# Optimization experiments

Measured on AMD Instinct MI355X. Metric: run time of the kernel, lower is better.

The kernel has to match this reference:

```python
import jax, jax.numpy as jnp
import numpy as np

B, C, IN, H = 64, 128, 1024, 512  # batch, channels, input features (=='seq_length' arg), hidden


def setup_inputs() -> dict:
    key = jax.random.key(0)
    ks = jax.random.split(key, 9)
    s = 1.0 / np.sqrt(H)  # PyTorch LSTM init: U(-1/sqrt(H), 1/sqrt(H))
    u = lambda k, shape: jax.random.uniform(k, shape, jnp.float32, -s, s)
    return {
        "x": jax.random.normal(ks[0], (B, C, IN), jnp.float32),
        # layer 0: one weight set per direction (fwd, bwd)
        "W_ih0": u(ks[1], (2, 4 * H, IN)),
        "W_hh0": u(ks[2], (2, 4 * H, H)),
        "b_ih0": u(ks[3], (2, 4 * H)),
        "b_hh0": u(ks[4], (2, 4 * H)),
        # layers 1..2: input is concat of both directions (2H)
        "W_ih12": u(ks[5], (2, 2, 4 * H, 2 * H)),
        "W_hh12": u(ks[6], (2, 2, 4 * H, H)),
        "b_ih12": u(ks[7], (2, 2, 4 * H)),
        "b_hh12": u(ks[8], (2, 2, 4 * H)),
    }


def _cell(inp, W_ih, b_ih, b_hh):
    # One LSTM step from zero state (h0 = c0 = 0): W_hh @ h0 == 0, f*c0 == 0.
    gates = inp @ W_ih.T + b_ih + b_hh  # [N, 4H]
    i, f, g, o = jnp.split(gates, 4, axis=-1)  # PyTorch gate order: i, f, g, o
    c = jax.nn.sigmoid(i) * jnp.tanh(g)
    return jax.nn.sigmoid(o) * jnp.tanh(c)  # h, shape [N, H]


def reference(x, W_ih0, W_hh0, b_ih0, b_hh0, W_ih12, W_hh12, b_ih12, b_hh12):
    b, c, n = x.shape
    # Each channel is an independent seq-len-1 LSTM call with zero init state,
    # so fold channels into the batch dimension. W_hh* contribute nothing (h0=0).
    xb = x.reshape(b * c, n)
    h = jnp.concatenate(
        [_cell(xb, W_ih0[d], b_ih0[d], b_hh0[d]) for d in range(2)], axis=-1
    )  # [b*c, 2H]
    for l in range(2):  # layers 1 and 2
        h = jnp.concatenate(
            [_cell(h, W_ih12[l, d], b_ih12[l, d], b_hh12[l, d]) for d in range(2)],
            axis=-1,
        )
    return h.reshape(b, c, 2 * H)  # [batch, channels, 2*hidden]
```

## Files before the change

### kernel.cpp

```cpp
#include <hip/hip_runtime.h>


typedef float f32x4 __attribute__((ext_vector_type(4)));
typedef short short8 __attribute__((ext_vector_type(8)));
typedef unsigned short u16;

#define NP 3072
#define MROWS 8192
#define KDIM 1024
#define BM 256
#define BN 192
#define BK 64
#define LDS_A_SZ (BM * BK * 2)
#define LDS_B_SZ (BN * BK * 2)
#define LDS_B_OFF (2 * LDS_A_SZ)

__device__ __forceinline__ u16 f2bf(float f) {
  unsigned u = __float_as_uint(f);
  u += 0x7fffu + ((u >> 16) & 1u);
  return (u16)(u >> 16);
}
__device__ __forceinline__ float sigmoid_f(float x) {
  return 1.0f / (1.0f + __expf(-x));
}
__device__ __forceinline__ float tanh_f(float x) {
  float xc = fminf(fmaxf(x, -15.0f), 15.0f);
  float e = __expf(2.0f * xc);
  return (e - 1.0f) / (e + 1.0f);
}
__device__ __forceinline__ void gload_lds16(const void* g, void* l) {
  __builtin_amdgcn_global_load_lds((const __attribute__((address_space(1))) void*)g,
                                   (__attribute__((address_space(3))) void*)l,
                                   16, 0, 0);
}


__global__ __launch_bounds__(256) void k_convert_x(const float* __restrict__ x,
                                                   u16* __restrict__ out) {
  int tid = blockIdx.x * 256 + threadIdx.x;
  const float4* src = (const float4*)x + (size_t)tid * 2;
  float4 v0 = src[0], v1 = src[1];
  union { u16 u[8]; uint4 v; } r;
  r.u[0] = f2bf(v0.x); r.u[1] = f2bf(v0.y); r.u[2] = f2bf(v0.z); r.u[3] = f2bf(v0.w);
  r.u[4] = f2bf(v1.x); r.u[5] = f2bf(v1.y); r.u[6] = f2bf(v1.z); r.u[7] = f2bf(v1.w);
  ((uint4*)out)[tid] = r.v;
}

__global__ __launch_bounds__(256) void k_pack_w(const float* __restrict__ Wih0,
                                                const float* __restrict__ Wih12,
                                                u16* __restrict__ P) {
  int tid = blockIdx.x * 256 + threadIdx.x;
  int s   = tid / (NP * 128);
  int rem = tid - s * (NP * 128);
  int p   = rem >> 7;
  int k8  = rem & 127;
  int hb = p / 48;
  int pr = p - hb * 48;
  int gs = pr >> 4;
  int hl = pr & 15;
  int hcol = hb * 16 + hl;
  int dir = hcol >> 9;
  int h   = hcol & 511;
  int og  = (gs == 0) ? 0 : (gs + 1);
  const float* src;
  if (s == 0)
    src = Wih0 + ((size_t)(dir * 2048 + og * 512 + h)) * 1024 + k8 * 8;
  else
    src = Wih12 + ((size_t)(((s - 1) * 2 + dir) * 2048 + og * 512 + h)) * 1024 + k8 * 8;
  float4 v0 = ((const float4*)src)[0];
  float4 v1 = ((const float4*)src)[1];
  union { u16 u[8]; uint4 v; } r;
  r.u[0] = f2bf(v0.x); r.u[1] = f2bf(v0.y); r.u[2] = f2bf(v0.z); r.u[3] = f2bf(v0.w);
  r.u[4] = f2bf(v1.x); r.u[5] = f2bf(v1.y); r.u[6] = f2bf(v1.z); r.u[7] = f2bf(v1.w);
  ((uint4*)P)[tid] = r.v;
}

__global__ __launch_bounds__(256) void k_pack_bias(const float* __restrict__ bih0,
                                                   const float* __restrict__ bhh0,
                                                   const float* __restrict__ bih12,
                                                   const float* __restrict__ bhh12,
                                                   float* __restrict__ pb) {
  int tid = blockIdx.x * 256 + threadIdx.x;
  if (tid >= 3 * NP) return;
  int s = tid / NP;
  int p = tid - s * NP;
  int hb = p / 48;
  int pr = p - hb * 48;
  int gs = pr >> 4;
  int hl = pr & 15;
  int hcol = hb * 16 + hl;
  int dir = hcol >> 9;
  int h   = hcol & 511;
  int og  = (gs == 0) ? 0 : (gs + 1);
  int j   = og * 512 + h;
  float v;
  if (s == 0) {
    int i = dir * 2048 + j;
    v = bih0[i] + bhh0[i];
  } else {
    int i = ((s - 1) * 2 + dir) * 2048 + j;
    v = bih12[i] + bhh12[i];
  }
  pb[tid] = v;
}


#define BAR()    __builtin_amdgcn_s_barrier()
#define SCHEDB() __builtin_amdgcn_sched_barrier(0)
#define WAITV(N) asm volatile("s_waitcnt vmcnt(" #N ")" ::: "memory")
#define MM(Macc, Aop, Bop) Macc = __builtin_amdgcn_mfma_f32_16x16x32_bf16(Aop, Bop, Macc, 0, 0, 0)

#define LDA(MQ, K32, M4, BUF) \
  (*(const short8*)(lds + ((K32) ? aK1 : aK0) + ((BUF) * LDS_A_SZ + (MQ) * 8192 + (M4) * 2048)))
#define LDB(N3, K32, BUF) \
  (*(const short8*)(lds + ((K32) ? bK1 : bK0) + ((BUF) * LDS_B_SZ + (N3) * 2048)))

#define STAGE_B(RB, BUF, KT) \
  gload_lds16(srcB + (size_t)(RB) * 64 * KDIM + (size_t)(KT) * BK, \
              lds + LDS_B_OFF + (BUF) * LDS_B_SZ + (RB) * 8192 + t * 16)
#define STAGE_A(ROWB, BUF, KT) \
  gload_lds16(srcA + (size_t)(ROWB) * KDIM + (size_t)(KT) * BK, \
              lds + (BUF) * LDS_A_SZ + (ROWB) * 128 + t * 16)

#define MM12(MQ, AA0, AA1, AA2, AA3, BB0, BB1, BB2) \
  MM(acc[(MQ)*4+0][0], AA0, BB0); MM(acc[(MQ)*4+1][0], AA1, BB0); \
  MM(acc[(MQ)*4+2][0], AA2, BB0); MM(acc[(MQ)*4+3][0], AA3, BB0); \
  MM(acc[(MQ)*4+0][1], AA0, BB1); MM(acc[(MQ)*4+1][1], AA1, BB1); \
  MM(acc[(MQ)*4+2][1], AA2, BB1); MM(acc[(MQ)*4+3][1], AA3, BB1); \
  MM(acc[(MQ)*4+0][2], AA0, BB2); MM(acc[(MQ)*4+1][2], AA1, BB2); \
  MM(acc[(MQ)*4+2][2], AA2, BB2); MM(acc[(MQ)*4+3][2], AA3, BB2);

#define TILE1(BUF, KT, DO_STAGE) \
  { \
    if (DO_STAGE) { STAGE_B(0, (BUF)^1, (KT)+1); STAGE_B(1, (BUF)^1, (KT)+1); STAGE_B(2, (BUF)^1, (KT)+1); \
                    STAGE_A(0, (BUF)^1, (KT)+1); STAGE_A(128, (BUF)^1, (KT)+1); \
                    STAGE_A(64, (BUF)^1, (KT)+1); STAGE_A(192, (BUF)^1, (KT)+1); } \
    SCHEDB(); \
    a0 = LDA(0, 0, 0, BUF); a1 = LDA(0, 0, 1, BUF); a2 = LDA(0, 0, 2, BUF); a3 = LDA(0, 0, 3, BUF); \
    b00 = LDB(0, 0, BUF); b01 = LDB(1, 0, BUF); b02 = LDB(2, 0, BUF); \
    a8 = LDA(1, 0, 0, BUF); a9 = LDA(1, 0, 1, BUF); aA = LDA(1, 0, 2, BUF); aB = LDA(1, 0, 3, BUF); \
    a4 = LDA(0, 1, 0, BUF); a5 = LDA(0, 1, 1, BUF); a6 = LDA(0, 1, 2, BUF); a7 = LDA(0, 1, 3, BUF); \
    b10 = LDB(0, 1, BUF); b11 = LDB(1, 1, BUF); b12 = LDB(2, 1, BUF); \
    aC = LDA(1, 1, 0, BUF); aD = LDA(1, 1, 1, BUF); aE = LDA(1, 1, 2, BUF); aF = LDA(1, 1, 3, BUF); \
    __builtin_amdgcn_s_setprio(1); \
    MM12(0, a0, a1, a2, a3, b00, b01, b02); \
    MM12(1, a8, a9, aA, aB, b00, b01, b02); \
    MM12(0, a4, a5, a6, a7, b10, b11, b12); \
    MM12(1, aC, aD, aE, aF, b10, b11, b12); \
    __builtin_amdgcn_s_setprio(0); \
    WAITV(0); \
    BAR(); SCHEDB(); \
  }

template <bool F32OUT>
__global__ __launch_bounds__(512, 2) void k_lstm_gemm8(const u16* __restrict__ A,
                                                       const u16* __restrict__ Bp,
                                                       const float* __restrict__ bias,
                                                       void* __restrict__ outp) {
  __shared__ __align__(16) char lds[114688];
  const int t    = threadIdx.x;
  const int lane = t & 63;
  const int w    = t >> 6;
  const int wr   = w >> 2;
  const int wc   = w & 3;
  const int r16  = lane & 15, kg = lane >> 4;

  const int n_hw = blockIdx.y * gridDim.x + blockIdx.x;
  const int c    = n_hw & 7;
  const int wlc  = n_hw >> 3;
  const int bx   = (c & 1) * 8 + (wlc & 7);
  const int by   = (c >> 1) * 8 + (wlc >> 3);
  const int brow = by * BM;
  const int bn0  = bx * BN;

  const int sw    = r16 & 7;
  const int slot0 = kg ^ sw;
  const int aK0 = wr * 16384 + r16 * 128 + slot0 * 16;
  const int aK1 = wr * 16384 + r16 * 128 + (slot0 ^ 4) * 16;
  const int bK0 = LDS_B_OFF + (wc * 48 + r16) * 128 + slot0 * 16;
  const int bK1 = LDS_B_OFF + (wc * 48 + r16) * 128 + (slot0 ^ 4) * 16;

  const int rr   = t >> 3;
  const int koct = ((t & 7) ^ (rr & 7)) << 3;
  const u16* srcA = A  + (size_t)(brow + rr) * KDIM + koct;
  const u16* srcB = Bp + (size_t)(bn0  + rr) * KDIM + koct;

  f32x4 acc[8][3];
#pragma unroll
  for (int m = 0; m < 8; ++m)
#pragma unroll
    for (int n = 0; n < 3; ++n) acc[m][n] = (f32x4){0.f, 0.f, 0.f, 0.f};

  short8 a0, a1, a2, a3, a4, a5, a6, a7, a8, a9, aA, aB, aC, aD, aE, aF;
  short8 b00, b01, b02, b10, b11, b12;

  STAGE_B(0, 0, 0); STAGE_B(1, 0, 0); STAGE_B(2, 0, 0);
  STAGE_A(0, 0, 0); STAGE_A(128, 0, 0);
  STAGE_A(64, 0, 0); STAGE_A(192, 0, 0);
  WAITV(0);
  BAR(); SCHEDB();

  for (int k2 = 0; k2 < 7; ++k2) {
    int kt = k2 * 2;
    TILE1(0, kt, 1);
    TILE1(1, kt + 1, 1);
  }
  TILE1(0, 14, 1);
  TILE1(1, 15, 0);

  {
    int pb = bn0 + wc * 48;
    float biV = bias[pb + r16];
    float bgV = bias[pb + 16 + r16];
    float boV = bias[pb + 32 + r16];
    int hcol = (bx * 4 + wc) * 16 + r16;
#pragma unroll
    for (int m8 = 0; m8 < 8; ++m8) {
      int rowb = brow + wr * 128 + (m8 >> 2) * 64 + (m8 & 3) * 16 + kg * 4;
#pragma unroll
      for (int r = 0; r < 4; ++r) {
        float vi = acc[m8][0][r] + biV;
        float vg = acc[m8][1][r] + bgV;
        float vo = acc[m8][2][r] + boV;
        float c2 = sigmoid_f(vi) * tanh_f(vg);
        float hv = sigmoid_f(vo) * tanh_f(c2);
        size_t oidx = (size_t)(rowb + r) * 1024 + hcol;
        if (F32OUT) ((float*)outp)[oidx] = hv;
        else        ((u16*)outp)[oidx]   = f2bf(hv);
      }
    }
  }
}

extern "C" void kernel_launch(void* const* d_in, const int* in_sizes, int n_in,
                              void* d_out, int out_size, void* d_ws, size_t ws_size,
                              hipStream_t stream) {
  const float* x     = (const float*)d_in[0];
  const float* Wih0  = (const float*)d_in[1];
  const float* bih0  = (const float*)d_in[3];
  const float* bhh0  = (const float*)d_in[4];
  const float* Wih12 = (const float*)d_in[5];
  const float* bih12 = (const float*)d_in[7];
  const float* bhh12 = (const float*)d_in[8];

  char* ws = (char*)d_ws;
  u16*   xbf = (u16*)ws;
  u16*   h1  = (u16*)(ws + 16777216);
  u16*   h2  = (u16*)(ws + 33554432);
  u16*   P3  = (u16*)(ws + 50331648);
  float* pb3 = (float*)(ws + 69206016);

  k_convert_x<<<4096, 256, 0, stream>>>(x, xbf);
  k_pack_w<<<4608, 256, 0, stream>>>(Wih0, Wih12, P3);
  k_pack_bias<<<36, 256, 0, stream>>>(bih0, bhh0, bih12, bhh12, pb3);

  dim3 grid(NP / BN, MROWS / BM);
  k_lstm_gemm8<false><<<grid, 512, 0, stream>>>(xbf, P3, pb3, h1);
  k_lstm_gemm8<false><<<grid, 512, 0, stream>>>(h1, P3 + (size_t)NP * KDIM, pb3 + NP, h2);
  k_lstm_gemm8<true ><<<grid, 512, 0, stream>>>(h2, P3 + (size_t)2 * NP * KDIM, pb3 + 2 * NP, d_out);
}
```

Before: 197.3 us.

## Load B operands directly from global into registers, stage only A in LDS

B-matrix fragments are now read straight from global memory into registers, double-buffered across the two K halves, instead of going through LDS. LDS holds only the A tile. Warps are remapped from a 2x4 to a 4x2 grid, so each warp computes 64 rows by 96 columns. This cuts LDS footprint and LDS read traffic, but adds global loads with latency the schedule must hide, raises register pressure, and can lower reuse of B across warps.

```diff
diff --git a/kernel.cpp b/kernel.cpp
--- a/kernel.cpp
+++ b/kernel.cpp
@@ -12,8 +12,6 @@
 #define BN 192
 #define BK 64
 #define LDS_A_SZ (BM * BK * 2)
-#define LDS_B_SZ (BN * BK * 2)
-#define LDS_B_OFF (2 * LDS_A_SZ)
 
 __device__ __forceinline__ u16 f2bf(float f) {
   unsigned u = __float_as_uint(f);
@@ -110,46 +108,54 @@
 #define WAITV(N) asm volatile("s_waitcnt vmcnt(" #N ")" ::: "memory")
 #define MM(Macc, Aop, Bop) Macc = __builtin_amdgcn_mfma_f32_16x16x32_bf16(Aop, Bop, Macc, 0, 0, 0)
 
-#define LDA(MQ, K32, M4, BUF) \
-  (*(const short8*)(lds + ((K32) ? aK1 : aK0) + ((BUF) * LDS_A_SZ + (MQ) * 8192 + (M4) * 2048)))
-#define LDB(N3, K32, BUF) \
-  (*(const short8*)(lds + ((K32) ? bK1 : bK0) + ((BUF) * LDS_B_SZ + (N3) * 2048)))
-
-#define STAGE_B(RB, BUF, KT) \
-  gload_lds16(srcB + (size_t)(RB) * 64 * KDIM + (size_t)(KT) * BK, \
-              lds + LDS_B_OFF + (BUF) * LDS_B_SZ + (RB) * 8192 + t * 16)
+#define LDA0(M4) (*(const short8*)(lds + aK0 + ((M4) * 2048)))
+#define LDA1(M4) (*(const short8*)(lds + aK1 + ((M4) * 2048)))
+#define LDA0B(M4) (*(const short8*)(lds + LDS_A_SZ + aK0 + ((M4) * 2048)))
+#define LDA1B(M4) (*(const short8*)(lds + LDS_A_SZ + aK1 + ((M4) * 2048)))
+
 #define STAGE_A(ROWB, BUF, KT) \
   gload_lds16(srcA + (size_t)(ROWB) * KDIM + (size_t)(KT) * BK, \
               lds + (BUF) * LDS_A_SZ + (ROWB) * 128 + t * 16)
-
-#define MM12(MQ, AA0, AA1, AA2, AA3, BB0, BB1, BB2) \
-  MM(acc[(MQ)*4+0][0], AA0, BB0); MM(acc[(MQ)*4+1][0], AA1, BB0); \
-  MM(acc[(MQ)*4+2][0], AA2, BB0); MM(acc[(MQ)*4+3][0], AA3, BB0); \
-  MM(acc[(MQ)*4+0][1], AA0, BB1); MM(acc[(MQ)*4+1][1], AA1, BB1); \
-  MM(acc[(MQ)*4+2][1], AA2, BB1); MM(acc[(MQ)*4+3][1], AA3, BB1); \
-  MM(acc[(MQ)*4+0][2], AA0, BB2); MM(acc[(MQ)*4+1][2], AA1, BB2); \
-  MM(acc[(MQ)*4+2][2], AA2, BB2); MM(acc[(MQ)*4+3][2], AA3, BB2);
-
-#define TILE1(BUF, KT, DO_STAGE) \
+#define STAGE_A4(BUF, KT) \
+  STAGE_A(0, BUF, KT); STAGE_A(64, BUF, KT); STAGE_A(128, BUF, KT); STAGE_A(192, BUF, KT)
+
+#define BLOAD6(DST, KT, K32) \
+  DST##0 = *(const short8*)(bB + 0 * 16 * KDIM + (KT) * 64 + (K32) * 32); \
+  DST##1 = *(const short8*)(bB + 1 * 16 * KDIM + (KT) * 64 + (K32) * 32); \
+  DST##2 = *(const short8*)(bB + 2 * 16 * KDIM + (KT) * 64 + (K32) * 32); \
+  DST##3 = *(const short8*)(bB + 3 * 16 * KDIM + (KT) * 64 + (K32) * 32); \
+  DST##4 = *(const short8*)(bB + 4 * 16 * KDIM + (KT) * 64 + (K32) * 32); \
+  DST##5 = *(const short8*)(bB + 5 * 16 * KDIM + (KT) * 64 + (K32) * 32)
+
+#define MM24(A0_, A1_, A2_, A3_, BB) \
+  MM(acc[0][0], A0_, BB##0); MM(acc[1][0], A1_, BB##0); MM(acc[2][0], A2_, BB##0); MM(acc[3][0], A3_, BB##0); \
+  MM(acc[0][1], A0_, BB##1); MM(acc[1][1], A1_, BB##1); MM(acc[2][1], A2_, BB##1); MM(acc[3][1], A3_, BB##1); \
+  MM(acc[0][2], A0_, BB##2); MM(acc[1][2], A1_, BB##2); MM(acc[2][2], A2_, BB##2); MM(acc[3][2], A3_, BB##2); \
+  MM(acc[0][3], A0_, BB##3); MM(acc[1][3], A1_, BB##3); MM(acc[2][3], A2_, BB##3); MM(acc[3][3], A3_, BB##3); \
+  MM(acc[0][4], A0_, BB##4); MM(acc[1][4], A1_, BB##4); MM(acc[2][4], A2_, BB##4); MM(acc[3][4], A3_, BB##4); \
+  MM(acc[0][5], A0_, BB##5); MM(acc[1][5], A1_, BB##5); MM(acc[2][5], A2_, BB##5); MM(acc[3][5], A3_, BB##5)
+
+#define TILE(BUF, KT, DO_STAGE) \
   { \
-    if (DO_STAGE) { STAGE_B(0, (BUF)^1, (KT)+1); STAGE_B(1, (BUF)^1, (KT)+1); STAGE_B(2, (BUF)^1, (KT)+1); \
-                    STAGE_A(0, (BUF)^1, (KT)+1); STAGE_A(128, (BUF)^1, (KT)+1); \
-                    STAGE_A(64, (BUF)^1, (KT)+1); STAGE_A(192, (BUF)^1, (KT)+1); } \
-    SCHEDB(); \
-    a0 = LDA(0, 0, 0, BUF); a1 = LDA(0, 0, 1, BUF); a2 = LDA(0, 0, 2, BUF); a3 = LDA(0, 0, 3, BUF); \
-    b00 = LDB(0, 0, BUF); b01 = LDB(1, 0, BUF); b02 = LDB(2, 0, BUF); \
-    a8 = LDA(1, 0, 0, BUF); a9 = LDA(1, 0, 1, BUF); aA = LDA(1, 0, 2, BUF); aB = LDA(1, 0, 3, BUF); \
-    a4 = LDA(0, 1, 0, BUF); a5 = LDA(0, 1, 1, BUF); a6 = LDA(0, 1, 2, BUF); a7 = LDA(0, 1, 3, BUF); \
-    b10 = LDB(0, 1, BUF); b11 = LDB(1, 1, BUF); b12 = LDB(2, 1, BUF); \
-    aC = LDA(1, 1, 0, BUF); aD = LDA(1, 1, 1, BUF); aE = LDA(1, 1, 2, BUF); aF = LDA(1, 1, 3, BUF); \
+    if (DO_STAGE) { STAGE_A4((BUF)^1, (KT)+1); } \
+    SCHEDB(); \
+    BLOAD6(bqA, KT, 1); \
+    SCHEDB(); \
+    if (BUF) { aA0 = LDA0B(0); aA1 = LDA0B(1); aA2 = LDA0B(2); aA3 = LDA0B(3); } \
+    else     { aA0 = LDA0(0);  aA1 = LDA0(1);  aA2 = LDA0(2);  aA3 = LDA0(3);  } \
     __builtin_amdgcn_s_setprio(1); \
-    MM12(0, a0, a1, a2, a3, b00, b01, b02); \
-    MM12(1, a8, a9, aA, aB, b00, b01, b02); \
-    MM12(0, a4, a5, a6, a7, b10, b11, b12); \
-    MM12(1, aC, aD, aE, aF, b10, b11, b12); \
+    MM24(aA0, aA1, aA2, aA3, bqB); \
     __builtin_amdgcn_s_setprio(0); \
-    WAITV(0); \
-    BAR(); SCHEDB(); \
+    SCHEDB(); \
+    if (DO_STAGE) { BLOAD6(bqB, (KT)+1, 0); } \
+    SCHEDB(); \
+    if (BUF) { aA0 = LDA1B(0); aA1 = LDA1B(1); aA2 = LDA1B(2); aA3 = LDA1B(3); } \
+    else     { aA0 = LDA1(0);  aA1 = LDA1(1);  aA2 = LDA1(2);  aA3 = LDA1(3);  } \
+    __builtin_amdgcn_s_setprio(1); \
+    MM24(aA0, aA1, aA2, aA3, bqA); \
+    __builtin_amdgcn_s_setprio(0); \
+    if (DO_STAGE) { WAITV(6); BAR(); } \
+    SCHEDB(); \
   }
 
 template <bool F32OUT>
@@ -157,12 +163,12 @@
                                                        const u16* __restrict__ Bp,
                                                        const float* __restrict__ bias,
                                                        void* __restrict__ outp) {
-  __shared__ __align__(16) char lds[114688];
+  __shared__ __align__(16) char lds[2 * LDS_A_SZ];
   const int t    = threadIdx.x;
   const int lane = t & 63;
   const int w    = t >> 6;
-  const int wr   = w >> 2;
-  const int wc   = w & 3;
+  const int wr   = w >> 1;
+  const int wc   = w & 1;
   const int r16  = lane & 15, kg = lane >> 4;
 
   const int n_hw = blockIdx.y * gridDim.x + blockIdx.x;
@@ -173,55 +179,53 @@
   const int brow = by * BM;
   const int bn0  = bx * BN;
 
-  const int sw    = r16 & 7;
-  const int slot0 = kg ^ sw;
-  const int aK0 = wr * 16384 + r16 * 128 + slot0 * 16;
-  const int aK1 = wr * 16384 + r16 * 128 + (slot0 ^ 4) * 16;
-  const int bK0 = LDS_B_OFF + (wc * 48 + r16) * 128 + slot0 * 16;
-  const int bK1 = LDS_B_OFF + (wc * 48 + r16) * 128 + (slot0 ^ 4) * 16;
+  const int slot0 = kg ^ (r16 & 7);
+  const int aK0 = wr * 8192 + r16 * 128 + slot0 * 16;
+  const int aK1 = wr * 8192 + r16 * 128 + (slot0 ^ 4) * 16;
 
   const int rr   = t >> 3;
   const int koct = ((t & 7) ^ (rr & 7)) << 3;
-  const u16* srcA = A  + (size_t)(brow + rr) * KDIM + koct;
-  const u16* srcB = Bp + (size_t)(bn0  + rr) * KDIM + koct;
-
-  f32x4 acc[8][3];
-#pragma unroll
-  for (int m = 0; m < 8; ++m)
-#pragma unroll
-    for (int n = 0; n < 3; ++n) acc[m][n] = (f32x4){0.f, 0.f, 0.f, 0.f};
-
-  short8 a0, a1, a2, a3, a4, a5, a6, a7, a8, a9, aA, aB, aC, aD, aE, aF;
-  short8 b00, b01, b02, b10, b11, b12;
-
-  STAGE_B(0, 0, 0); STAGE_B(1, 0, 0); STAGE_B(2, 0, 0);
-  STAGE_A(0, 0, 0); STAGE_A(128, 0, 0);
-  STAGE_A(64, 0, 0); STAGE_A(192, 0, 0);
-  WAITV(0);
+  const u16* srcA = A + (size_t)(brow + rr) * KDIM + koct;
+
+  const u16* bB = Bp + (size_t)(bn0 + wc * 96 + r16) * KDIM + kg * 8;
+
+  f32x4 acc[4][6];
+#pragma unroll
+  for (int m = 0; m < 4; ++m)
+#pragma unroll
+    for (int n = 0; n < 6; ++n) acc[m][n] = (f32x4){0.f, 0.f, 0.f, 0.f};
+
+  short8 aA0, aA1, aA2, aA3;
+  short8 bqA0, bqA1, bqA2, bqA3, bqA4, bqA5;
+  short8 bqB0, bqB1, bqB2, bqB3, bqB4, bqB5;
+
+  STAGE_A4(0, 0);
+  SCHEDB();
+  BLOAD6(bqB, 0, 0);
+  SCHEDB();
+  WAITV(6);
   BAR(); SCHEDB();
 
-  for (int k2 = 0; k2 < 7; ++k2) {
-    int kt = k2 * 2;
-    TILE1(0, kt, 1);
-    TILE1(1, kt + 1, 1);
-  }
-  TILE1(0, 14, 1);
-  TILE1(1, 15, 0);
-
-  {
-    int pb = bn0 + wc * 48;
-    float biV = bias[pb + r16];
-    float bgV = bias[pb + 16 + r16];
-    float boV = bias[pb + 32 + r16];
-    int hcol = (bx * 4 + wc) * 16 + r16;
-#pragma unroll
-    for (int m8 = 0; m8 < 8; ++m8) {
-      int rowb = brow + wr * 128 + (m8 >> 2) * 64 + (m8 & 3) * 16 + kg * 4;
+  TILE(0, 0, 1);  TILE(1, 1, 1);  TILE(0, 2, 1);  TILE(1, 3, 1);
+  TILE(0, 4, 1);  TILE(1, 5, 1);  TILE(0, 6, 1);  TILE(1, 7, 1);
+  TILE(0, 8, 1);  TILE(1, 9, 1);  TILE(0, 10, 1); TILE(1, 11, 1);
+  TILE(0, 12, 1); TILE(1, 13, 1); TILE(0, 14, 1); TILE(1, 15, 0);
+
+#pragma unroll
+  for (int hb2 = 0; hb2 < 2; ++hb2) {
+    int pbase = bn0 + wc * 96 + hb2 * 48;
+    float biV = bias[pbase + r16];
+    float bgV = bias[pbase + 16 + r16];
+    float boV = bias[pbase + 32 + r16];
+    int hcol = (pbase / 48) * 16 + r16;
+#pragma unroll
+    for (int m = 0; m < 4; ++m) {
+      int rowb = brow + wr * 64 + m * 16 + kg * 4;
 #pragma unroll
       for (int r = 0; r < 4; ++r) {
-        float vi = acc[m8][0][r] + biV;
-        float vg = acc[m8][1][r] + bgV;
-        float vo = acc[m8][2][r] + boV;
+        float vi = acc[m][hb2 * 3 + 0][r] + biV;
+        float vg = acc[m][hb2 * 3 + 1][r] + bgV;
+        float vo = acc[m][hb2 * 3 + 2][r] + boV;
         float c2 = sigmoid_f(vi) * tanh_f(vg);
         float hv = sigmoid_f(vo) * tanh_f(c2);
         size_t oidx = (size_t)(rowb + r) * 1024 + hcol;
```

New measurement: 359.9 us. 82.4% more time.
